# Performance work log

Measured on AMD Instinct MI355X. Metric: run time of the kernel, lower is better.

Reference implementation:

```python
import jax, jax.numpy as jnp
import numpy as np

N_NODES = 100000
N_EDGES = 3200000
F_IN = 256
HIDDEN = 16
N_CLASSES = 32


def setup_inputs() -> dict:
    key = jax.random.key(0)
    ks = jax.random.split(key, 9)
    x = jax.random.normal(ks[0], (N_NODES, F_IN), dtype=jnp.float32)
    edge_index = jax.random.randint(ks[1], (2, N_EDGES), 0, N_NODES)
    edge_attr = jax.random.uniform(ks[2], (N_EDGES, 1), dtype=jnp.float32)
    s1 = 1.0 / np.sqrt(F_IN)
    W1 = jax.random.normal(ks[3], (2, F_IN, HIDDEN), dtype=jnp.float32) * s1
    root1 = jax.random.normal(ks[4], (F_IN, HIDDEN), dtype=jnp.float32) * s1
    bias1 = jnp.zeros((HIDDEN,), dtype=jnp.float32)
    s2 = 1.0 / np.sqrt(HIDDEN)
    W2 = jax.random.normal(ks[5], (2, HIDDEN, N_CLASSES), dtype=jnp.float32) * s2
    root2 = jax.random.normal(ks[6], (HIDDEN, N_CLASSES), dtype=jnp.float32) * s2
    bias2 = jnp.zeros((N_CLASSES,), dtype=jnp.float32)
    return {"x": x, "edge_attr": edge_attr, "W1": W1, "root1": root1,
            "bias1": bias1, "W2": W2, "root2": root2, "bias2": bias2,
            "edge_index": edge_index}


def spline_conv(x, src, dst, u, W, root, bias):
    """SplineConv, dim=1, kernel_size=2, degree=1, open spline, aggr='mean'.

    With K=2 and degree-1 open splines, v = u*(K-1) = u, so the B-spline basis
    per edge is simply ((1-u), u) over kernel weights W[0], W[1].
    """
    n = x.shape[0]
    # Node-level GEMMs once (cheaper than per-edge F_IN-dim gathers): [2, N, out]
    xs = jnp.einsum('nf,kfo->kno', x, W)
    # Per-edge basis-weighted message from source nodes: [E, out]
    msg = (1.0 - u)[:, None] * xs[0, src] + u[:, None] * xs[1, src]
    agg = jax.ops.segment_sum(msg, dst, num_segments=n)
    cnt = jax.ops.segment_sum(jnp.ones((dst.shape[0],), x.dtype), dst,
                              num_segments=n)
    return agg / jnp.maximum(cnt, 1.0)[:, None] + x @ root + bias


def reference(x, edge_attr, W1, root1, bias1, W2, root2, bias2, edge_index):
    src, dst = edge_index[0], edge_index[1]
    u = jnp.clip(edge_attr[:, 0], 0.0, 1.0)  # pseudo coords in [0, 1]
    # dropout with training=False is identity (eval-mode reference)
    h = jax.nn.elu(spline_conv(x, src, dst, u, W1, root1, bias1))
    out = spline_conv(h, src, dst, u, W2, root2, bias2)
    return jax.nn.log_softmax(out, axis=1)
```

## Files before the change

### kernel.cpp

```cpp
#include <hip/hip_runtime.h>
#include <hip/hip_fp16.h>
#include <math.h>

#define NN 100000
#define NE 3200000
#define FIN 256
#define HID 16
#define NC 32
#define NBUK 782
#define CAP 5120
#define SC_BLOCKS 250
#define SC_TILE 12800
#define SC_EPT 13

typedef __attribute__((ext_vector_type(8))) short short8;
typedef __attribute__((ext_vector_type(4))) float f32x4;
typedef union { uint4 u; short8 s; } U8;

#define RU(r) ((float)((r) >> 24) * (1.f / 255.f))

__global__ __launch_bounds__(256) void k_prepB(
    const float* __restrict__ W1, const float* __restrict__ root1,
    uint4* __restrict__ Bpk)
{
    int idx = blockIdx.x * 256 + threadIdx.x;
    if (idx >= 1536) return;
    int c = idx & 15, kc = (idx >> 4) & 31, t = idx >> 9;
    unsigned hi[8], lo[8];
    #pragma unroll
    for (int e = 0; e < 8; ++e) {
        int k = kc * 8 + e;
        float v;
        if (t == 0)      v = W1[k * 16 + c];
        else if (t == 1) v = W1[FIN * 16 + k * 16 + c];
        else             v = root1[k * 16 + c];
        unsigned u = __float_as_uint(v);
        unsigned h = u & 0xFFFF0000u;
        float lf = v - __uint_as_float(h);
        hi[e] = h;
        lo[e] = __float_as_uint(lf) & 0xFFFF0000u;
    }
    uint4 H, L;
    H.x = (hi[0] >> 16) | hi[1];  H.y = (hi[2] >> 16) | hi[3];
    H.z = (hi[4] >> 16) | hi[5];  H.w = (hi[6] >> 16) | hi[7];
    L.x = (lo[0] >> 16) | lo[1];  L.y = (lo[2] >> 16) | lo[3];
    L.z = (lo[4] >> 16) | lo[5];  L.w = (lo[6] >> 16) | lo[7];
    Bpk[(size_t)idx * 2]     = H;
    Bpk[(size_t)idx * 2 + 1] = L;
}

__global__ __launch_bounds__(256) void k_gemm1(
    const float* __restrict__ x, const uint4* __restrict__ Bpk,
    const float* __restrict__ bias1,
    __half2* __restrict__ xs1p, __half2* __restrict__ r1h)
{
    int wid = (blockIdx.x << 2) + (threadIdx.x >> 6);
    if (wid >= NN / 16) return;
    int lane = threadIdx.x & 63;
    int c = lane & 15, kcl = lane >> 4;
    int n0 = wid * 16;

    const float* xr = x + (size_t)(n0 + c) * FIN + kcl * 8;
    f32x4 acc0 = {0.f, 0.f, 0.f, 0.f};
    f32x4 acc1 = {0.f, 0.f, 0.f, 0.f};
    f32x4 acc2 = {0.f, 0.f, 0.f, 0.f};

    #define PACK(f0, f1, HO, LO) {                                     \
        unsigned u0 = __float_as_uint(f0), u1 = __float_as_uint(f1);   \
        unsigned h0 = u0 & 0xFFFF0000u, h1 = u1 & 0xFFFF0000u;         \
        HO = (h0 >> 16) | h1;                                          \
        float l0 = (f0) - __uint_as_float(h0);                         \
        float l1 = (f1) - __uint_as_float(h1);                         \
        LO = (__float_as_uint(l0) >> 16) |                             \
             (__float_as_uint(l1) & 0xFFFF0000u); }

    #pragma unroll
    for (int s = 0; s < 8; ++s) {
        float4 a0 = *(const float4*)(xr + s * 32);
        float4 a1 = *(const float4*)(xr + s * 32 + 4);
        U8 ahi, alo;
        PACK(a0.x, a0.y, ahi.u.x, alo.u.x)
        PACK(a0.z, a0.w, ahi.u.y, alo.u.y)
        PACK(a1.x, a1.y, ahi.u.z, alo.u.z)
        PACK(a1.z, a1.w, ahi.u.w, alo.u.w)

        const uint4* bp = Bpk + ((size_t)((s * 4 + kcl) * 16 + c)) * 2;
        U8 bh0, bl0, bh1, bl1, bh2, bl2;
        bh0.u = bp[0];     bl0.u = bp[1];
        bh1.u = bp[1024];  bl1.u = bp[1025];
        bh2.u = bp[2048];  bl2.u = bp[2049];

        acc0 = __builtin_amdgcn_mfma_f32_16x16x32_bf16(ahi.s, bh0.s, acc0, 0, 0, 0);
        acc0 = __builtin_amdgcn_mfma_f32_16x16x32_bf16(alo.s, bh0.s, acc0, 0, 0, 0);
        acc0 = __builtin_amdgcn_mfma_f32_16x16x32_bf16(ahi.s, bl0.s, acc0, 0, 0, 0);
        acc1 = __builtin_amdgcn_mfma_f32_16x16x32_bf16(ahi.s, bh1.s, acc1, 0, 0, 0);
        acc1 = __builtin_amdgcn_mfma_f32_16x16x32_bf16(alo.s, bh1.s, acc1, 0, 0, 0);
        acc1 = __builtin_amdgcn_mfma_f32_16x16x32_bf16(ahi.s, bl1.s, acc1, 0, 0, 0);
        acc2 = __builtin_amdgcn_mfma_f32_16x16x32_bf16(ahi.s, bh2.s, acc2, 0, 0, 0);
        acc2 = __builtin_amdgcn_mfma_f32_16x16x32_bf16(alo.s, bh2.s, acc2, 0, 0, 0);
        acc2 = __builtin_amdgcn_mfma_f32_16x16x32_bf16(ahi.s, bl2.s, acc2, 0, 0, 0);
    }
    #undef PACK

    #pragma unroll
    for (int r = 0; r < 4; ++r) {
        int n = n0 + kcl * 4 + r;
        xs1p[(size_t)n * 16 + c] = __floats2half2_rn(acc0[r], acc1[r]);
    }
    float b = bias1[c];
    #pragma unroll
    for (int r = 0; r < 4; ++r) {
        int n = n0 + kcl * 4 + r;
        float v = acc2[r] + b;
        float vo = __shfl_xor(v, 1, 64);
        if (!(c & 1))
            r1h[(size_t)n * 8 + (c >> 1)] = __floats2half2_rn(v, vo);
    }
}

__global__ __launch_bounds__(1024) void k_binscatter(
    const int* __restrict__ ei, const float* __restrict__ ea,
    int* __restrict__ gcnt, unsigned* __restrict__ rec)
{
    __shared__ unsigned sbuf[SC_TILE];
    __shared__ int cnt[NBUK], gb[NBUK], cur[NBUK];
    __shared__ int ss[1024];
    int t = threadIdx.x;
    if (t < NBUK) cnt[t] = 0;
    __syncthreads();

    int e0 = blockIdx.x * SC_TILE;
    int   dl[SC_EPT];
    int   sl[SC_EPT];
    float ul[SC_EPT];
    #pragma unroll
    for (int k = 0; k < SC_EPT; ++k) {
        int i = t + k * 1024;
        if (i < SC_TILE) {
            dl[k] = ei[NE + e0 + i];
            sl[k] = ei[e0 + i];
            ul[k] = ea[e0 + i];
            atomicAdd(&cnt[dl[k] >> 7], 1);
        }
    }
    __syncthreads();

    int v = (t < NBUK) ? cnt[t] : 0;
    ss[t] = v;
    __syncthreads();
    for (int off = 1; off < 1024; off <<= 1) {
        int a = (t >= off) ? ss[t - off] : 0;
        __syncthreads();
        ss[t] += a;
        __syncthreads();
    }
    if (t < NBUK) {
        int lbase = ss[t] - v;
        cur[t] = lbase;
        if (v) gb[t] = t * CAP + atomicAdd(&gcnt[t], v) - lbase;
    }
    __syncthreads();

    #pragma unroll
    for (int k = 0; k < SC_EPT; ++k) {
        int i = t + k * 1024;
        if (i < SC_TILE) {
            float u = fminf(fmaxf(ul[k], 0.f), 1.f);
            unsigned uq = (unsigned)(u * 255.f + 0.5f);
            int pos = atomicAdd(&cur[dl[k] >> 7], 1);
            sbuf[pos] = (unsigned)sl[k] | ((unsigned)(dl[k] & 127) << 17)
                      | (uq << 24);
        }
    }
    __syncthreads();

    int wid = t >> 6, lane = t & 63;
    for (int b = wid; b < NBUK; b += 16) {
        int n_ = cnt[b];
        if (!n_) continue;
        int lb = cur[b] - n_;
        int gbb = gb[b];
        for (int i = lane; i < n_; i += 64)
            rec[gbb + lb + i] = sbuf[lb + i];
    }
}

__global__ __launch_bounds__(512) void k_agg1s(
    const int* __restrict__ gcnt, const unsigned* __restrict__ rec,
    const uint4* __restrict__ xs4, const __half2* __restrict__ r1h,
    __half2* __restrict__ hh2)
{
    __shared__ unsigned sbv[CAP];
    __shared__ int cnt[128], cur[128];
    int t = threadIdx.x;
    if (t < 128) cnt[t] = 0;
    __syncthreads();

    int b = blockIdx.x;
    int base = b * CAP, m = gcnt[b];
    for (int i = t; i < m; i += 512)
        atomicAdd(&cnt[(rec[base + i] >> 17) & 127], 1);
    __syncthreads();
    if (t < 64) {
        int c0 = cnt[2 * t], c1 = cnt[2 * t + 1];
        int sp = c0 + c1, v = sp;
        #pragma unroll
        for (int off = 1; off < 64; off <<= 1) {
            int o = __shfl_up(v, off, 64);
            if (t >= off) v += o;
        }
        int excl = v - sp;
        cur[2 * t] = excl;
        cur[2 * t + 1] = excl + c0;
    }
    __syncthreads();
    for (int i = t; i < m; i += 512) {
        unsigned v = rec[base + i];
        int p = atomicAdd(&cur[(v >> 17) & 127], 1);
        sbv[p] = v;
    }
    __syncthreads();

    int nl = t >> 2, j = t & 3;
    int d = cnt[nl];
    int e = cur[nl], s = e - d;

    float a0 = 0.f, a1 = 0.f, a2 = 0.f, a3 = 0.f;
    #define ACC1(r_, g) {                                           \
        float u = RU(r_);                                           \
        float w0 = 1.f - u;                                         \
        const __half2* hp_ = (const __half2*)&(g);                  \
        float2 f0 = __half22float2(hp_[0]);                         \
        float2 f1 = __half22float2(hp_[1]);                         \
        float2 f2 = __half22float2(hp_[2]);                         \
        float2 f3 = __half22float2(hp_[3]);                         \
        a0 += w0 * f0.x + u * f0.y;                                 \
        a1 += w0 * f1.x + u * f1.y;                                 \
        a2 += w0 * f2.x + u * f2.y;                                 \
        a3 += w0 * f3.x + u * f3.y; }

    int k = s;
    for (; k + 8 <= e; k += 8) {
        unsigned q[8]; uint4 g[8];
        #pragma unroll
        for (int z = 0; z < 8; ++z) q[z] = sbv[k + z];
        #pragma unroll
        for (int z = 0; z < 8; ++z) g[z] = xs4[(size_t)(q[z] & 0x1FFFF) * 4 + j];
        #pragma unroll
        for (int z = 0; z < 8; ++z) { ACC1(q[z], g[z]) }
    }
    for (; k < e; ++k) {
        unsigned q = sbv[k];
        uint4 g = xs4[(size_t)(q & 0x1FFFF) * 4 + j];
        ACC1(q, g)
    }
    #undef ACC1

    int n = b * 128 + nl;
    if (n < NN) {
        float inv = 1.f / fmaxf((float)d, 1.f);
        float2 rrA = __half22float2(r1h[(size_t)n * 8 + 2 * j]);
        float2 rrB = __half22float2(r1h[(size_t)n * 8 + 2 * j + 1]);
        float v0 = a0 * inv + rrA.x;
        float v1 = a1 * inv + rrA.y;
        float v2 = a2 * inv + rrB.x;
        float v3 = a3 * inv + rrB.y;
        v0 = v0 > 0.f ? v0 : expm1f(v0);
        v1 = v1 > 0.f ? v1 : expm1f(v1);
        v2 = v2 > 0.f ? v2 : expm1f(v2);
        v3 = v3 > 0.f ? v3 : expm1f(v3);
        hh2[(size_t)n * 8 + 2 * j]     = __floats2half2_rn(v0, v1);
        hh2[(size_t)n * 8 + 2 * j + 1] = __floats2half2_rn(v2, v3);
    }
}

__global__ __launch_bounds__(512) void k_agg2s(
    const int* __restrict__ gcnt, const unsigned* __restrict__ rec,
    const uint4* __restrict__ hh4, const __half2* __restrict__ hh,
    const float* __restrict__ W2, const float* __restrict__ root2,
    const float* __restrict__ bias2, float* __restrict__ out)
{
    __shared__ float wsm[1568];
    __shared__ unsigned sbv[CAP];
    __shared__ float hv[128 * 18];
    __shared__ int cnt[128], cur[128];
    int t = threadIdx.x;
    for (int i = t; i < 1568; i += 512)
        wsm[i] = (i < 1024) ? W2[i] : (i < 1536 ? root2[i - 1024] : bias2[i - 1536]);
    if (t < 128) cnt[t] = 0;
    __syncthreads();

    int b = blockIdx.x;
    int base = b * CAP, m = gcnt[b];
    for (int i = t; i < m; i += 512)
        atomicAdd(&cnt[(rec[base + i] >> 17) & 127], 1);
    __syncthreads();
    if (t < 64) {
        int c0 = cnt[2 * t], c1 = cnt[2 * t + 1];
        int sp = c0 + c1, v = sp;
        #pragma unroll
        for (int off = 1; off < 64; off <<= 1) {
            int o = __shfl_up(v, off, 64);
            if (t >= off) v += o;
        }
        int excl = v - sp;
        cur[2 * t] = excl;
        cur[2 * t + 1] = excl + c0;
    }
    __syncthreads();
    for (int i = t; i < m; i += 512) {
        unsigned v = rec[base + i];
        int p = atomicAdd(&cur[(v >> 17) & 127], 1);
        sbv[p] = v;
    }
    __syncthreads();

    int nl = t >> 2, j = (t >> 1) & 1, h = t & 1;
    int d = cnt[nl];
    int e = cur[nl], s = e - d;

    float s0[8], s1[8];
    #pragma unroll
    for (int w = 0; w < 8; ++w) { s0[w] = 0.f; s1[w] = 0.f; }

    #define ACC2(r_, g) {                                           \
        float u = RU(r_);                                           \
        float w0 = 1.f - u;                                         \
        const __half2* hp_ = (const __half2*)&(g);                  \
        _Pragma("unroll")                                           \
        for (int w = 0; w < 4; ++w) {                               \
            float2 f = __half22float2(hp_[w]);                      \
            s0[2*w]   += w0 * f.x; s1[2*w]   += u * f.x;            \
            s0[2*w+1] += w0 * f.y; s1[2*w+1] += u * f.y;            \
        } }

    int k = s + h;
    for (; k + 8 <= e; k += 8) {
        unsigned q[4]; uint4 g[4];
        #pragma unroll
        for (int z = 0; z < 4; ++z) q[z] = sbv[k + 2 * z];
        #pragma unroll
        for (int z = 0; z < 4; ++z) g[z] = hh4[(size_t)(q[z] & 0x1FFFF) * 2 + j];
        #pragma unroll
        for (int z = 0; z < 4; ++z) { ACC2(q[z], g[z]) }
    }
    for (; k < e; k += 2) {
        unsigned q = sbv[k];
        uint4 g = hh4[(size_t)(q & 0x1FFFF) * 2 + j];
        ACC2(q, g)
    }
    #undef ACC2

    #pragma unroll
    for (int w = 0; w < 8; ++w) {
        s0[w] += __shfl_xor(s0[w], 1, 64);
        s1[w] += __shfl_xor(s1[w], 1, 64);
    }

    __syncthreads();
    float* ssm = (float*)sbv;
    if (h == 0) {
        #pragma unroll
        for (int w = 0; w < 8; ++w) {
            ssm[nl * 33 + 8 * j + w]      = s0[w];
            ssm[nl * 33 + 16 + 8 * j + w] = s1[w];
        }
    }
    int j4 = t & 3;
    int n = b * 128 + nl;
    bool valid = n < NN;
    if (valid) {
        uint2 gh = ((const uint2*)hh)[(size_t)n * 4 + j4];
        float2 h0 = __half22float2(*(const __half2*)&gh.x);
        float2 h1 = __half22float2(*(const __half2*)&gh.y);
        hv[nl * 18 + 4 * j4]     = h0.x;
        hv[nl * 18 + 4 * j4 + 1] = h0.y;
        hv[nl * 18 + 4 * j4 + 2] = h1.x;
        hv[nl * 18 + 4 * j4 + 3] = h1.y;
    } else {
        hv[nl * 18 + 4 * j4]     = 0.f;
        hv[nl * 18 + 4 * j4 + 1] = 0.f;
        hv[nl * 18 + 4 * j4 + 2] = 0.f;
        hv[nl * 18 + 4 * j4 + 3] = 0.f;
    }
    if (j4 == 0) hv[nl * 18 + 16] = 1.f / fmaxf((float)d, 1.f);
    __syncthreads();

    float invn = hv[nl * 18 + 16];
    float v[8];
    #pragma unroll
    for (int cc = 0; cc < 8; ++cc) {
        int c = j4 * 8 + cc;
        float acc = wsm[1536 + c];
        float agg = 0.f;
        #pragma unroll
        for (int kk = 0; kk < 16; ++kk) {
            agg += ssm[nl * 33 + kk] * wsm[kk * 32 + c]
                 + ssm[nl * 33 + 16 + kk] * wsm[512 + kk * 32 + c];
            acc += hv[nl * 18 + kk] * wsm[1024 + kk * 32 + c];
        }
        v[cc] = acc + agg * invn;
    }

    float mx = v[0];
    #pragma unroll
    for (int cc = 1; cc < 8; ++cc) mx = fmaxf(mx, v[cc]);
    #pragma unroll
    for (int off = 1; off < 4; off <<= 1)
        mx = fmaxf(mx, __shfl_xor(mx, off, 4));
    float sm = 0.f;
    #pragma unroll
    for (int cc = 0; cc < 8; ++cc) sm += expf(v[cc] - mx);
    #pragma unroll
    for (int off = 1; off < 4; off <<= 1)
        sm += __shfl_xor(sm, off, 4);
    float ls = mx + logf(sm);
    if (valid) {
        float4* op = (float4*)(out + (size_t)n * 32 + j4 * 8);
        op[0] = make_float4(v[0] - ls, v[1] - ls, v[2] - ls, v[3] - ls);
        op[1] = make_float4(v[4] - ls, v[5] - ls, v[6] - ls, v[7] - ls);
    }
}

extern "C" void kernel_launch(void* const* d_in, const int* in_sizes, int n_in,
                              void* d_out, int out_size, void* d_ws, size_t ws_size,
                              hipStream_t stream)
{
    const float* x     = (const float*)d_in[0];
    const float* ea    = (const float*)d_in[1];
    const float* W1    = (const float*)d_in[2];
    const float* root1 = (const float*)d_in[3];
    const float* bias1 = (const float*)d_in[4];
    const float* W2    = (const float*)d_in[5];
    const float* root2 = (const float*)d_in[6];
    const float* bias2 = (const float*)d_in[7];
    const int*   ei    = (const int*)d_in[8];
    float* out = (float*)d_out;

    float* ws = (float*)d_ws;
    __half2* xs1p = (__half2*)ws;
    __half2* r1h  = (__half2*)(ws + (size_t)NN * 16);
    __half2* hh2  = (__half2*)(ws + (size_t)NN * 24);
    unsigned* rec = (unsigned*)(ws + (size_t)NN * 32);
    int*     gcnt = (int*)(ws + (size_t)NN * 32 + (size_t)NBUK * CAP);
    uint4* Bpk = (uint4*)(ws + (size_t)NN * 24);

    hipMemsetAsync(gcnt, 0, NBUK * sizeof(int), stream);

    k_prepB<<<6, 256, 0, stream>>>(W1, root1, Bpk);
    k_gemm1<<<(NN / 16 + 3) / 4, 256, 0, stream>>>(x, Bpk, bias1, xs1p, r1h);
    k_binscatter<<<SC_BLOCKS, 1024, 0, stream>>>(ei, ea, gcnt, rec);
    k_agg1s<<<NBUK, 512, 0, stream>>>(gcnt, rec, (const uint4*)xs1p, r1h, hh2);
    k_agg2s<<<NBUK, 512, 0, stream>>>(gcnt, rec, (const uint4*)hh2, hh2,
                                      W2, root2, bias2, out);
}
```

Baseline: 337.7 us.

## Reuse per-bucket node sort from layer 1 in layer 2, double scatter blocks

The first aggregation kernel now writes its in-shared-memory counting sort of edge records back to global memory, along with per-node start and end offsets. The second aggregation kernel then skips its own histogram, scan and atomic scatter and just loads the pre-sorted records. This adds a global write of the records and of two offset arrays in layer 1. Separately, the bin-scatter kernel runs twice as many blocks, each with half the tile size.

```diff
diff --git a/kernel.cpp b/kernel.cpp
--- a/kernel.cpp
+++ b/kernel.cpp
@@ -9,9 +9,9 @@
 #define NC 32
 #define NBUK 782
 #define CAP 5120
-#define SC_BLOCKS 250
-#define SC_TILE 12800
-#define SC_EPT 13
+#define SC_BLOCKS 500
+#define SC_TILE 6400
+#define SC_EPT 7
 
 typedef __attribute__((ext_vector_type(8))) short short8;
 typedef __attribute__((ext_vector_type(4))) float f32x4;
@@ -186,9 +186,10 @@
 }
 
 __global__ __launch_bounds__(512) void k_agg1s(
-    const int* __restrict__ gcnt, const unsigned* __restrict__ rec,
+    const int* __restrict__ gcnt, unsigned* __restrict__ rec,
     const uint4* __restrict__ xs4, const __half2* __restrict__ r1h,
-    __half2* __restrict__ hh2)
+    __half2* __restrict__ hh2, int* __restrict__ rstart,
+    int* __restrict__ rend)
 {
     __shared__ unsigned sbv[CAP];
     __shared__ int cnt[128], cur[128];
@@ -220,6 +221,15 @@
         sbv[p] = v;
     }
     __syncthreads();
+
+    for (int i = t; i < m; i += 512) rec[base + i] = sbv[i];
+    if (t < 128) {
+        int n = b * 128 + t;
+        if (n < NN) {
+            rstart[n] = cur[t] - cnt[t];
+            rend[n]   = cur[t];
+        }
+    }
 
     int nl = t >> 2, j = t & 3;
     int d = cnt[nl];
@@ -277,47 +287,28 @@
 __global__ __launch_bounds__(512) void k_agg2s(
     const int* __restrict__ gcnt, const unsigned* __restrict__ rec,
     const uint4* __restrict__ hh4, const __half2* __restrict__ hh,
+    const int* __restrict__ rstart, const int* __restrict__ rend,
     const float* __restrict__ W2, const float* __restrict__ root2,
     const float* __restrict__ bias2, float* __restrict__ out)
 {
     __shared__ float wsm[1568];
     __shared__ unsigned sbv[CAP];
     __shared__ float hv[128 * 18];
-    __shared__ int cnt[128], cur[128];
     int t = threadIdx.x;
     for (int i = t; i < 1568; i += 512)
         wsm[i] = (i < 1024) ? W2[i] : (i < 1536 ? root2[i - 1024] : bias2[i - 1536]);
-    if (t < 128) cnt[t] = 0;
-    __syncthreads();
 
     int b = blockIdx.x;
     int base = b * CAP, m = gcnt[b];
-    for (int i = t; i < m; i += 512)
-        atomicAdd(&cnt[(rec[base + i] >> 17) & 127], 1);
-    __syncthreads();
-    if (t < 64) {
-        int c0 = cnt[2 * t], c1 = cnt[2 * t + 1];
-        int sp = c0 + c1, v = sp;
-        #pragma unroll
-        for (int off = 1; off < 64; off <<= 1) {
-            int o = __shfl_up(v, off, 64);
-            if (t >= off) v += o;
-        }
-        int excl = v - sp;
-        cur[2 * t] = excl;
-        cur[2 * t + 1] = excl + c0;
-    }
-    __syncthreads();
-    for (int i = t; i < m; i += 512) {
-        unsigned v = rec[base + i];
-        int p = atomicAdd(&cur[(v >> 17) & 127], 1);
-        sbv[p] = v;
-    }
-    __syncthreads();
+    for (int i = t; i < m; i += 512) sbv[i] = rec[base + i];
 
     int nl = t >> 2, j = (t >> 1) & 1, h = t & 1;
-    int d = cnt[nl];
-    int e = cur[nl], s = e - d;
+    int n = b * 128 + nl;
+    bool valid = n < NN;
+    int s = 0, e = 0;
+    if (valid) { s = rstart[n]; e = rend[n]; }
+    int d = e - s;
+    __syncthreads();
 
     float s0[8], s1[8];
     #pragma unroll
@@ -367,8 +358,6 @@
         }
     }
     int j4 = t & 3;
-    int n = b * 128 + nl;
-    bool valid = n < NN;
     if (valid) {
         uint2 gh = ((const uint2*)hh)[(size_t)n * 4 + j4];
         float2 h0 = __half22float2(*(const __half2*)&gh.x);
@@ -442,7 +431,10 @@
     __half2* r1h  = (__half2*)(ws + (size_t)NN * 16);
     __half2* hh2  = (__half2*)(ws + (size_t)NN * 24);
     unsigned* rec = (unsigned*)(ws + (size_t)NN * 32);
-    int*     gcnt = (int*)(ws + (size_t)NN * 32 + (size_t)NBUK * CAP);
+    int*     iws  = (int*)(ws + (size_t)NN * 32 + (size_t)NBUK * CAP);
+    int* gcnt   = iws;
+    int* rstart = iws + NBUK;
+    int* rend   = iws + NBUK + NN;
     uint4* Bpk = (uint4*)(ws + (size_t)NN * 24);
 
     hipMemsetAsync(gcnt, 0, NBUK * sizeof(int), stream);
@@ -450,7 +442,8 @@
     k_prepB<<<6, 256, 0, stream>>>(W1, root1, Bpk);
     k_gemm1<<<(NN / 16 + 3) / 4, 256, 0, stream>>>(x, Bpk, bias1, xs1p, r1h);
     k_binscatter<<<SC_BLOCKS, 1024, 0, stream>>>(ei, ea, gcnt, rec);
-    k_agg1s<<<NBUK, 512, 0, stream>>>(gcnt, rec, (const uint4*)xs1p, r1h, hh2);
+    k_agg1s<<<NBUK, 512, 0, stream>>>(gcnt, rec, (const uint4*)xs1p, r1h, hh2,
+                                      rstart, rend);
     k_agg2s<<<NBUK, 512, 0, stream>>>(gcnt, rec, (const uint4*)hh2, hh2,
-                                      W2, root2, bias2, out);
-}
+                                      rstart, rend, W2, root2, bias2, out);
+}
```

Result: no change. 342.9 us (+1.5%).
